# Optimization experiments

Measured on AMD Instinct MI355X. Metric: run time of the kernel, lower is better.

The kernel has to match this reference:

```python
import jax, jax.numpy as jnp
import numpy as np

EMBED_DIM = 1024
NUM_HEADS = 16
HEAD_DIM = EMBED_DIM // NUM_HEADS


def setup_inputs() -> dict:
    key = jax.random.key(0)
    ks = jax.random.split(key, 6)
    s = 1.0 / np.sqrt(EMBED_DIM)
    x = jax.random.normal(ks[0], (2, 2048, EMBED_DIM), dtype=jnp.float32)
    Wk = jax.random.uniform(ks[1], (EMBED_DIM, EMBED_DIM), jnp.float32, -s, s)
    Wq = jax.random.uniform(ks[2], (EMBED_DIM, EMBED_DIM), jnp.float32, -s, s)
    Wv = jax.random.uniform(ks[3], (EMBED_DIM, EMBED_DIM), jnp.float32, -s, s)
    Wo = jax.random.uniform(ks[4], (EMBED_DIM, EMBED_DIM), jnp.float32, -s, s)
    bo = jax.random.uniform(ks[5], (EMBED_DIM,), jnp.float32, -s, s)
    return {"x": x, "Wq": Wq, "Wk": Wk, "Wv": Wv, "Wo": Wo, "bo": bo}


def reference(x, Wq, Wk, Wv, Wo, bo):
    b, s, e = x.shape
    h, d = NUM_HEADS, HEAD_DIM
    scale = d ** (-0.5)
    # nn.Linear: y = x @ W.T ; here W stored as [out, in] -> use W.T
    q = (x @ Wq.T).reshape(b, s, h, d).transpose(0, 2, 1, 3)  # b h s d
    k = (x @ Wk.T).reshape(b, s, h, d).transpose(0, 2, 1, 3)
    v = (x @ Wv.T).reshape(b, s, h, d).transpose(0, 2, 1, 3)
    logits = jnp.einsum('bhqd,bhkd->bhqk', q, k) * scale
    attn = jax.nn.softmax(logits, axis=-1)
    out = jnp.einsum('bhqk,bhkd->bhqd', attn, v)
    out = out.transpose(0, 2, 1, 3).reshape(b, s, e)
    return out @ Wo.T + bo
```

## Files before the change

kernel.cpp:

```cpp
#include <hip/hip_runtime.h>
#include <hip/hip_bf16.h>

using short8 = __attribute__((ext_vector_type(8))) short;
using f32x4  = __attribute__((ext_vector_type(4))) float;
using uint4v = __attribute__((ext_vector_type(4))) unsigned;

#if __has_builtin(__builtin_amdgcn_exp2f)
#define EXP2(x) __builtin_amdgcn_exp2f(x)
#else
#define EXP2(x) exp2f(x)
#endif

__device__ __forceinline__ short f2bf(float f) {
    union { float f; unsigned u; } v; v.f = f;
    unsigned r = v.u + 0x7fffu + ((v.u >> 16) & 1u);
    return (short)(r >> 16);
}
__device__ __forceinline__ unsigned pack_trunc(float a, float b) {
    union { float f; unsigned u; } ua, ub; ua.f = a; ub.f = b;
#if __has_builtin(__builtin_amdgcn_perm)
    return __builtin_amdgcn_perm(ub.u, ua.u, 0x07060302u);
#else
    return (ub.u & 0xFFFF0000u) | (ua.u >> 16);
#endif
}
__device__ __forceinline__ void async_copy16(const short* g, short* s) {
    __builtin_amdgcn_global_load_lds(
        (const __attribute__((address_space(1))) void*)g,
        (__attribute__((address_space(3))) void*)s, 16, 0, 0);
}

__global__ __launch_bounds__(256) void cvt_f32_bf16(
    const float* __restrict__ s0, const float* __restrict__ s1,
    const float* __restrict__ s2, const float* __restrict__ s3,
    const float* __restrict__ s4,
    short* __restrict__ d0, short* __restrict__ d1, short* __restrict__ d2,
    short* __restrict__ d3, short* __restrict__ d4,
    int n0, int n1, int n2, int n3, int n4) {
    const float* s; short* d; int n;
    switch (blockIdx.y) {
        case 0: s = s0; d = d0; n = n0; break;
        case 1: s = s1; d = d1; n = n1; break;
        case 2: s = s2; d = d2; n = n2; break;
        case 3: s = s3; d = d3; n = n3; break;
        default: s = s4; d = d4; n = n4; break;
    }
    const int idx = (blockIdx.x * 256 + threadIdx.x) * 4;
    if (idx < n) {
        float4 v = *(const float4*)(s + idx);
        short4 o;
        o.x = f2bf(v.x); o.y = f2bf(v.y); o.z = f2bf(v.z); o.w = f2bf(v.w);
        *(short4*)(d + idx) = o;
    }
}

template <int MODE, typename OT>
__device__ __forceinline__ void gemm_body(const short* __restrict__ A,
                                          const short* __restrict__ B,
                                          OT* __restrict__ C,
                                          const float* __restrict__ bias,
                                          float scale) {
    constexpr int Kd = 1024, Nd = 1024, Sd = 2048;
    __shared__ __align__(16) short As[128 * 32];
    __shared__ __align__(16) short Bs[128 * 32];

    const int tid  = threadIdx.x;
    const int w    = tid >> 6, lane = tid & 63;
    const int quad = lane >> 4, l16 = lane & 15;
    const int wm   = (w >> 1) * 64, wn = (w & 1) * 64;
    const int bm   = blockIdx.y * 128, bn = blockIdx.x * 128;

    f32x4 acc[4][4];
#pragma unroll
    for (int i = 0; i < 4; ++i)
#pragma unroll
        for (int j = 0; j < 4; ++j) acc[i][j] = (f32x4){0.f, 0.f, 0.f, 0.f};

    for (int k0 = 0; k0 < Kd; k0 += 32) {
        __syncthreads();
#pragma unroll
        for (int c = 0; c < 2; ++c) {
            int li  = c * 256 + tid;
            int row = li >> 2;
            int col = (li & 3) * 8;
            async_copy16(A + (size_t)(bm + row) * Kd + k0 + col, &As[li * 8]);
            async_copy16(B + (size_t)(bn + row) * Kd + k0 + col, &Bs[li * 8]);
        }
        __syncthreads();

        short8 af[4], bfv[4];
#pragma unroll
        for (int mi = 0; mi < 4; ++mi)
            af[mi] = *(const short8*)(&As[(wm + mi * 16 + l16) * 32 + quad * 8]);
#pragma unroll
        for (int ni = 0; ni < 4; ++ni)
            bfv[ni] = *(const short8*)(&Bs[(wn + ni * 16 + l16) * 32 + quad * 8]);
#pragma unroll
        for (int mi = 0; mi < 4; ++mi)
#pragma unroll
            for (int ni = 0; ni < 4; ++ni) {
                if constexpr (MODE == 2)
                    acc[mi][ni] = __builtin_amdgcn_mfma_f32_16x16x32_bf16(
                        bfv[ni], af[mi], acc[mi][ni], 0, 0, 0);
                else
                    acc[mi][ni] = __builtin_amdgcn_mfma_f32_16x16x32_bf16(
                        af[mi], bfv[ni], acc[mi][ni], 0, 0, 0);
            }
    }

    if constexpr (MODE == 2) {
#pragma unroll
        for (int mi = 0; mi < 4; ++mi) {
            const int m_g = bm + wm + mi * 16 + l16;
            const int b_  = m_g >> 11, s_ = m_g & 2047;
#pragma unroll
            for (int ni = 0; ni < 4; ++ni)
#pragma unroll
                for (int r = 0; r < 4; ++r) {
                    const int n_g = bn + wn + ni * 16 + quad * 4 + r;
                    C[(size_t)b_ * Nd * Sd + (size_t)n_g * Sd + s_] =
                        f2bf(acc[mi][ni][r]);
                }
        }
    } else {
#pragma unroll
        for (int ni = 0; ni < 4; ++ni) {
            const int colg = bn + wn + ni * 16 + l16;
            const float bv = (MODE == 1) ? bias[colg] : 0.f;
#pragma unroll
            for (int mi = 0; mi < 4; ++mi)
#pragma unroll
                for (int r = 0; r < 4; ++r) {
                    const int rowg = bm + wm + mi * 16 + quad * 4 + r;
                    if constexpr (MODE == 0)
                        C[(size_t)rowg * Nd + colg] = f2bf(acc[mi][ni][r] * scale);
                    else
                        C[(size_t)rowg * Nd + colg] = acc[mi][ni][r] + bv;
                }
        }
    }
}

#define CSC 0.18033688f

__global__ __launch_bounds__(256, 2) void proj_gemm(
    const short* __restrict__ X,
    const short* __restrict__ Wq, const short* __restrict__ Wk,
    const short* __restrict__ Wv,
    short* __restrict__ Qo, short* __restrict__ Ko, short* __restrict__ VTo) {
    if (blockIdx.z == 0)
        gemm_body<0, short>(X, Wq, Qo, nullptr, CSC);
    else if (blockIdx.z == 1)
        gemm_body<0, short>(X, Wk, Ko, nullptr, 1.0f);
    else
        gemm_body<2, short>(X, Wv, VTo, nullptr, 1.0f);
}

__global__ __launch_bounds__(256, 2) void out_gemm(
    const short* __restrict__ A, const short* __restrict__ W,
    const float* __restrict__ bias, float* __restrict__ C) {
    gemm_body<1, float>(A, W, C, bias, 1.0f);
}

__global__ __launch_bounds__(256, 2) void attn_kernel(
    const short* __restrict__ Q, const short* __restrict__ K,
    const short* __restrict__ VT, short* __restrict__ O) {
    constexpr int S = 2048, E = 1024, NT = S / 64;
    __shared__ __align__(16) short Ks[2][64 * 64];
    __shared__ __align__(16) short Vs[2][64 * 64];

    const int tid  = threadIdx.x;
    const int w    = tid >> 6, lane = tid & 63;
    const int quad = lane >> 4, l16 = lane & 15;
    const int bh   = blockIdx.y, b = bh >> 4, h = bh & 15;
    const int qt   = blockIdx.x;

    const int    q0   = qt * 128 + w * 32;
    const size_t base = (size_t)b * S * E;
    const size_t vtb  = (size_t)b * E * S;
    const int    hc   = h * 64;
    const int    xr   = l16 & 7;

    short8 aq[2][2];
#pragma unroll
    for (int qg = 0; qg < 2; ++qg) {
        const short* qp = Q + base + (size_t)(q0 + qg * 16 + l16) * E + hc + quad * 8;
        aq[qg][0] = *(const short8*)(qp);
        aq[qg][1] = *(const short8*)(qp + 32);
    }

    f32x4 oT[2][4], o_sum[2];
#pragma unroll
    for (int qg = 0; qg < 2; ++qg) {
        o_sum[qg] = (f32x4){0.f, 0.f, 0.f, 0.f};
#pragma unroll
        for (int i = 0; i < 4; ++i) oT[qg][i] = (f32x4){0.f, 0.f, 0.f, 0.f};
    }

    int          kdst[2], vdst0[2], vdst1[2];
    const short* kga[2];
    const short* vga[2];
#pragma unroll
    for (int c = 0; c < 2; ++c) {
        int li = c * 256 + tid, row = li >> 3, cc = li & 7;
        kdst[c] = row * 64 + ((cc ^ (row & 7)) * 8);
        int c0   = 4 * (cc >> 2) + 2 * (cc & 1);
        int boff = 4 * ((cc >> 1) & 1);
        vdst0[c] = row * 64 + ((c0 ^ (row & 7)) * 8) + boff;
        vdst1[c] = row * 64 + (((c0 + 1) ^ (row & 7)) * 8) + boff;
        kga[c]   = K + base + (size_t)row * E + hc + cc * 8;
        vga[c]   = VT + vtb + (size_t)(hc + row) * S + cc * 8;
    }

    short8 kr[2], vr[2];
#pragma unroll
    for (int c = 0; c < 2; ++c) {
        kr[c] = *(const short8*)(kga[c]);
        vr[c] = *(const short8*)(vga[c]);
    }
#pragma unroll
    for (int c = 0; c < 2; ++c) {
        *(short8*)(&Ks[0][kdst[c]]) = kr[c];
        short4 lo, hi;
        lo.x = vr[c][0]; lo.y = vr[c][1]; lo.z = vr[c][2]; lo.w = vr[c][3];
        hi.x = vr[c][4]; hi.y = vr[c][5]; hi.z = vr[c][6]; hi.w = vr[c][7];
        *(short4*)(&Vs[0][vdst0[c]]) = lo;
        *(short4*)(&Vs[0][vdst1[c]]) = hi;
    }
#pragma unroll
    for (int c = 0; c < 2; ++c) {
        kr[c] = *(const short8*)(kga[c] + (size_t)64 * E);
        vr[c] = *(const short8*)(vga[c] + 64);
    }
    __syncthreads();

    const short8 ones = (short8){0x3F80, 0x3F80, 0x3F80, 0x3F80,
                                 0x3F80, 0x3F80, 0x3F80, 0x3F80};
    const float  LB   = 0.00281502f;

    for (int kt = 0; kt < NT; ++kt) {
        const int    cur = kt & 1;
        const short* Kc  = Ks[cur];
        const short* Vc  = Vs[cur];

        if (kt + 1 < NT) {
            short* Kn = Ks[cur ^ 1];
            short* Vn = Vs[cur ^ 1];
#pragma unroll
            for (int c = 0; c < 2; ++c) {
                *(short8*)(&Kn[kdst[c]]) = kr[c];
                short4 lo, hi;
                lo.x = vr[c][0]; lo.y = vr[c][1]; lo.z = vr[c][2]; lo.w = vr[c][3];
                hi.x = vr[c][4]; hi.y = vr[c][5]; hi.z = vr[c][6]; hi.w = vr[c][7];
                *(short4*)(&Vn[vdst0[c]]) = lo;
                *(short4*)(&Vn[vdst1[c]]) = hi;
            }
            if (kt + 2 < NT) {
#pragma unroll
                for (int c = 0; c < 2; ++c) {
                    kr[c] = *(const short8*)(kga[c] + (size_t)(kt + 2) * 64 * E);
                    vr[c] = *(const short8*)(vga[c] + (kt + 2) * 64);
                }
            }
        }

        uint4v pkv[2][2];
#pragma unroll
        for (int kn = 0; kn < 4; ++kn) {
            const short* kb  = &Kc[(kn * 16 + l16) * 64];
            short8       bk0 = *(const short8*)(kb + ((quad ^ xr) * 8));
            short8       bk1 = *(const short8*)(kb + (((quad + 4) ^ xr) * 8));
#pragma unroll
            for (int qg = 0; qg < 2; ++qg) {
                f32x4 a = (f32x4){LB, LB, LB, LB};
                a = __builtin_amdgcn_mfma_f32_16x16x32_bf16(bk0, aq[qg][0], a, 0, 0, 0);
                a = __builtin_amdgcn_mfma_f32_16x16x32_bf16(bk1, aq[qg][1], a, 0, 0, 0);
                pkv[qg][kn >> 1][(kn & 1) * 2]     = pack_trunc(EXP2(a[0]), EXP2(a[1]));
                pkv[qg][kn >> 1][(kn & 1) * 2 + 1] = pack_trunc(EXP2(a[2]), EXP2(a[3]));
            }
        }

#pragma unroll
        for (int ks = 0; ks < 2; ++ks) {
            short8 pf[2];
#pragma unroll
            for (int qg = 0; qg < 2; ++qg) {
                union { uint4v u; short8 s; } cv;
                cv.u   = pkv[qg][ks];
                pf[qg] = cv.s;
                o_sum[qg] = __builtin_amdgcn_mfma_f32_16x16x32_bf16(
                    ones, pf[qg], o_sum[qg], 0, 0, 0);
            }
#pragma unroll
            for (int ni = 0; ni < 4; ++ni) {
                const int rv = ni * 16 + l16;
                short8 vb =
                    *(const short8*)(&Vc[rv * 64 + (((ks * 4 + quad) ^ xr) * 8)]);
#pragma unroll
                for (int qg = 0; qg < 2; ++qg)
                    oT[qg][ni] = __builtin_amdgcn_mfma_f32_16x16x32_bf16(
                        vb, pf[qg], oT[qg][ni], 0, 0, 0);
            }
        }
        __syncthreads();
    }

#pragma unroll
    for (int qg = 0; qg < 2; ++qg) {
        const float inv = 1.0f / o_sum[qg][0];
        const int   qg_ = q0 + qg * 16 + l16;
#pragma unroll
        for (int ni = 0; ni < 4; ++ni) {
            short4 ov;
            ov.x = f2bf(oT[qg][ni][0] * inv);
            ov.y = f2bf(oT[qg][ni][1] * inv);
            ov.z = f2bf(oT[qg][ni][2] * inv);
            ov.w = f2bf(oT[qg][ni][3] * inv);
            *(short4*)(&O[base + (size_t)qg_ * E + hc + ni * 16 + quad * 4]) = ov;
        }
    }
}

extern "C" void kernel_launch(void* const* d_in, const int* in_sizes, int n_in,
                              void* d_out, int out_size, void* d_ws, size_t ws_size,
                              hipStream_t stream) {
    const float* x  = (const float*)d_in[0];
    const float* Wq = (const float*)d_in[1];
    const float* Wk = (const float*)d_in[2];
    const float* Wv = (const float*)d_in[3];
    const float* Wo = (const float*)d_in[4];
    const float* bo = (const float*)d_in[5];
    float* out = (float*)d_out;

    constexpr int XN = 2 * 2048 * 1024;
    constexpr int WN = 1024 * 1024;

    short* Xb  = (short*)d_ws;
    short* Wqb = Xb + XN;
    short* Wkb = Wqb + WN;
    short* Wvb = Wkb + WN;
    short* Wob = Wvb + WN;
    short* Qb  = Wob + WN;
    short* Kb  = Qb + XN;
    short* VTb = Kb + XN;

    cvt_f32_bf16<<<dim3(4096, 5), 256, 0, stream>>>(
        x, Wq, Wk, Wv, Wo, Xb, Wqb, Wkb, Wvb, Wob, XN, WN, WN, WN, WN);
    proj_gemm<<<dim3(8, 32, 3), 256, 0, stream>>>(Xb, Wqb, Wkb, Wvb, Qb, Kb, VTb);
    attn_kernel<<<dim3(16, 32), 256, 0, stream>>>(Qb, Kb, VTb, Xb );
    out_gemm<<<dim3(8, 32, 1), 256, 0, stream>>>(Xb, Wob, bo, out);
}
```

Baseline: 178.9 us.

## Widen per-wave query tile in attention and retile output GEMM to 64x128

```diff
diff --git a/kernel.cpp b/kernel.cpp
--- a/kernel.cpp
+++ b/kernel.cpp
@@ -54,11 +54,10 @@
     }
 }
 
-template <int MODE, typename OT>
+template <int MODE>
 __device__ __forceinline__ void gemm_body(const short* __restrict__ A,
                                           const short* __restrict__ B,
-                                          OT* __restrict__ C,
-                                          const float* __restrict__ bias,
+                                          short* __restrict__ C,
                                           float scale) {
     constexpr int Kd = 1024, Nd = 1024, Sd = 2048;
     __shared__ __align__(16) short As[128 * 32];
@@ -126,16 +125,12 @@
 #pragma unroll
         for (int ni = 0; ni < 4; ++ni) {
             const int colg = bn + wn + ni * 16 + l16;
-            const float bv = (MODE == 1) ? bias[colg] : 0.f;
 #pragma unroll
             for (int mi = 0; mi < 4; ++mi)
 #pragma unroll
                 for (int r = 0; r < 4; ++r) {
                     const int rowg = bm + wm + mi * 16 + quad * 4 + r;
-                    if constexpr (MODE == 0)
-                        C[(size_t)rowg * Nd + colg] = f2bf(acc[mi][ni][r] * scale);
-                    else
-                        C[(size_t)rowg * Nd + colg] = acc[mi][ni][r] + bv;
+                    C[(size_t)rowg * Nd + colg] = f2bf(acc[mi][ni][r] * scale);
                 }
         }
     }
@@ -149,20 +144,77 @@
     const short* __restrict__ Wv,
     short* __restrict__ Qo, short* __restrict__ Ko, short* __restrict__ VTo) {
     if (blockIdx.z == 0)
-        gemm_body<0, short>(X, Wq, Qo, nullptr, CSC);
+        gemm_body<0>(X, Wq, Qo, CSC);
     else if (blockIdx.z == 1)
-        gemm_body<0, short>(X, Wk, Ko, nullptr, 1.0f);
+        gemm_body<0>(X, Wk, Ko, 1.0f);
     else
-        gemm_body<2, short>(X, Wv, VTo, nullptr, 1.0f);
+        gemm_body<2>(X, Wv, VTo, 1.0f);
 }
 
 __global__ __launch_bounds__(256, 2) void out_gemm(
-    const short* __restrict__ A, const short* __restrict__ W,
+    const short* __restrict__ A, const short* __restrict__ B,
     const float* __restrict__ bias, float* __restrict__ C) {
-    gemm_body<1, float>(A, W, C, bias, 1.0f);
-}
-
-__global__ __launch_bounds__(256, 2) void attn_kernel(
+    constexpr int Kd = 1024, Nd = 1024;
+    __shared__ __align__(16) short As[64 * 32];
+    __shared__ __align__(16) short Bs[128 * 32];
+
+    const int tid  = threadIdx.x;
+    const int w    = tid >> 6, lane = tid & 63;
+    const int quad = lane >> 4, l16 = lane & 15;
+    const int wm   = (w >> 1) * 32, wn = (w & 1) * 64;
+    const int bm   = blockIdx.y * 64, bn = blockIdx.x * 128;
+
+    f32x4 acc[2][4];
+#pragma unroll
+    for (int i = 0; i < 2; ++i)
+#pragma unroll
+        for (int j = 0; j < 4; ++j) acc[i][j] = (f32x4){0.f, 0.f, 0.f, 0.f};
+
+    for (int k0 = 0; k0 < Kd; k0 += 32) {
+        __syncthreads();
+        {
+            int row = tid >> 2, col = (tid & 3) * 8;
+            async_copy16(A + (size_t)(bm + row) * Kd + k0 + col, &As[tid * 8]);
+        }
+#pragma unroll
+        for (int c = 0; c < 2; ++c) {
+            int li  = c * 256 + tid;
+            int row = li >> 2;
+            int col = (li & 3) * 8;
+            async_copy16(B + (size_t)(bn + row) * Kd + k0 + col, &Bs[li * 8]);
+        }
+        __syncthreads();
+
+        short8 af[2], bfv[4];
+#pragma unroll
+        for (int mi = 0; mi < 2; ++mi)
+            af[mi] = *(const short8*)(&As[(wm + mi * 16 + l16) * 32 + quad * 8]);
+#pragma unroll
+        for (int ni = 0; ni < 4; ++ni)
+            bfv[ni] = *(const short8*)(&Bs[(wn + ni * 16 + l16) * 32 + quad * 8]);
+#pragma unroll
+        for (int mi = 0; mi < 2; ++mi)
+#pragma unroll
+            for (int ni = 0; ni < 4; ++ni)
+                acc[mi][ni] = __builtin_amdgcn_mfma_f32_16x16x32_bf16(
+                    af[mi], bfv[ni], acc[mi][ni], 0, 0, 0);
+    }
+
+#pragma unroll
+    for (int ni = 0; ni < 4; ++ni) {
+        const int colg = bn + wn + ni * 16 + l16;
+        const float bv = bias[colg];
+#pragma unroll
+        for (int mi = 0; mi < 2; ++mi)
+#pragma unroll
+            for (int r = 0; r < 4; ++r) {
+                const int rowg = bm + wm + mi * 16 + quad * 4 + r;
+                C[(size_t)rowg * Nd + colg] = acc[mi][ni][r] + bv;
+            }
+    }
+}
+
+__global__ __launch_bounds__(128, 1) void attn_kernel(
     const short* __restrict__ Q, const short* __restrict__ K,
     const short* __restrict__ VT, short* __restrict__ O) {
     constexpr int S = 2048, E = 1024, NT = S / 64;
@@ -175,34 +227,34 @@
     const int bh   = blockIdx.y, b = bh >> 4, h = bh & 15;
     const int qt   = blockIdx.x;
 
-    const int    q0   = qt * 128 + w * 32;
+    const int    q0   = qt * 128 + w * 64;
     const size_t base = (size_t)b * S * E;
     const size_t vtb  = (size_t)b * E * S;
     const int    hc   = h * 64;
     const int    xr   = l16 & 7;
 
-    short8 aq[2][2];
-#pragma unroll
-    for (int qg = 0; qg < 2; ++qg) {
+    short8 aq[4][2];
+#pragma unroll
+    for (int qg = 0; qg < 4; ++qg) {
         const short* qp = Q + base + (size_t)(q0 + qg * 16 + l16) * E + hc + quad * 8;
         aq[qg][0] = *(const short8*)(qp);
         aq[qg][1] = *(const short8*)(qp + 32);
     }
 
-    f32x4 oT[2][4], o_sum[2];
-#pragma unroll
-    for (int qg = 0; qg < 2; ++qg) {
+    f32x4 oT[4][4], o_sum[4];
+#pragma unroll
+    for (int qg = 0; qg < 4; ++qg) {
         o_sum[qg] = (f32x4){0.f, 0.f, 0.f, 0.f};
 #pragma unroll
         for (int i = 0; i < 4; ++i) oT[qg][i] = (f32x4){0.f, 0.f, 0.f, 0.f};
     }
 
-    int          kdst[2], vdst0[2], vdst1[2];
-    const short* kga[2];
-    const short* vga[2];
-#pragma unroll
-    for (int c = 0; c < 2; ++c) {
-        int li = c * 256 + tid, row = li >> 3, cc = li & 7;
+    int          kdst[4], vdst0[4], vdst1[4];
+    const short* kga[4];
+    const short* vga[4];
+#pragma unroll
+    for (int c = 0; c < 4; ++c) {
+        int li = c * 128 + tid, row = li >> 3, cc = li & 7;
         kdst[c] = row * 64 + ((cc ^ (row & 7)) * 8);
         int c0   = 4 * (cc >> 2) + 2 * (cc & 1);
         int boff = 4 * ((cc >> 1) & 1);
@@ -212,14 +264,14 @@
         vga[c]   = VT + vtb + (size_t)(hc + row) * S + cc * 8;
     }
 
-    short8 kr[2], vr[2];
-#pragma unroll
-    for (int c = 0; c < 2; ++c) {
+    short8 kr[4], vr[4];
+#pragma unroll
+    for (int c = 0; c < 4; ++c) {
         kr[c] = *(const short8*)(kga[c]);
         vr[c] = *(const short8*)(vga[c]);
     }
 #pragma unroll
-    for (int c = 0; c < 2; ++c) {
+    for (int c = 0; c < 4; ++c) {
         *(short8*)(&Ks[0][kdst[c]]) = kr[c];
         short4 lo, hi;
         lo.x = vr[c][0]; lo.y = vr[c][1]; lo.z = vr[c][2]; lo.w = vr[c][3];
@@ -228,7 +280,7 @@
         *(short4*)(&Vs[0][vdst1[c]]) = hi;
     }
 #pragma unroll
-    for (int c = 0; c < 2; ++c) {
+    for (int c = 0; c < 4; ++c) {
         kr[c] = *(const short8*)(kga[c] + (size_t)64 * E);
         vr[c] = *(const short8*)(vga[c] + 64);
     }
@@ -247,7 +299,7 @@
             short* Kn = Ks[cur ^ 1];
             short* Vn = Vs[cur ^ 1];
 #pragma unroll
-            for (int c = 0; c < 2; ++c) {
+            for (int c = 0; c < 4; ++c) {
                 *(short8*)(&Kn[kdst[c]]) = kr[c];
                 short4 lo, hi;
                 lo.x = vr[c][0]; lo.y = vr[c][1]; lo.z = vr[c][2]; lo.w = vr[c][3];
@@ -257,21 +309,21 @@
             }
             if (kt + 2 < NT) {
 #pragma unroll
-                for (int c = 0; c < 2; ++c) {
+                for (int c = 0; c < 4; ++c) {
                     kr[c] = *(const short8*)(kga[c] + (size_t)(kt + 2) * 64 * E);
                     vr[c] = *(const short8*)(vga[c] + (kt + 2) * 64);
                 }
             }
         }
 
-        uint4v pkv[2][2];
+        uint4v pkv[4][2];
 #pragma unroll
         for (int kn = 0; kn < 4; ++kn) {
             const short* kb  = &Kc[(kn * 16 + l16) * 64];
             short8       bk0 = *(const short8*)(kb + ((quad ^ xr) * 8));
             short8       bk1 = *(const short8*)(kb + (((quad + 4) ^ xr) * 8));
 #pragma unroll
-            for (int qg = 0; qg < 2; ++qg) {
+            for (int qg = 0; qg < 4; ++qg) {
                 f32x4 a = (f32x4){LB, LB, LB, LB};
                 a = __builtin_amdgcn_mfma_f32_16x16x32_bf16(bk0, aq[qg][0], a, 0, 0, 0);
                 a = __builtin_amdgcn_mfma_f32_16x16x32_bf16(bk1, aq[qg][1], a, 0, 0, 0);
@@ -282,9 +334,9 @@
 
 #pragma unroll
         for (int ks = 0; ks < 2; ++ks) {
-            short8 pf[2];
-#pragma unroll
-            for (int qg = 0; qg < 2; ++qg) {
+            short8 pf[4];
+#pragma unroll
+            for (int qg = 0; qg < 4; ++qg) {
                 union { uint4v u; short8 s; } cv;
                 cv.u   = pkv[qg][ks];
                 pf[qg] = cv.s;
@@ -297,7 +349,7 @@
                 short8 vb =
                     *(const short8*)(&Vc[rv * 64 + (((ks * 4 + quad) ^ xr) * 8)]);
 #pragma unroll
-                for (int qg = 0; qg < 2; ++qg)
+                for (int qg = 0; qg < 4; ++qg)
                     oT[qg][ni] = __builtin_amdgcn_mfma_f32_16x16x32_bf16(
                         vb, pf[qg], oT[qg][ni], 0, 0, 0);
             }
@@ -306,7 +358,7 @@
     }
 
 #pragma unroll
-    for (int qg = 0; qg < 2; ++qg) {
+    for (int qg = 0; qg < 4; ++qg) {
         const float inv = 1.0f / o_sum[qg][0];
         const int   qg_ = q0 + qg * 16 + l16;
 #pragma unroll
@@ -347,6 +399,6 @@
     cvt_f32_bf16<<<dim3(4096, 5), 256, 0, stream>>>(
         x, Wq, Wk, Wv, Wo, Xb, Wqb, Wkb, Wvb, Wob, XN, WN, WN, WN, WN);
     proj_gemm<<<dim3(8, 32, 3), 256, 0, stream>>>(Xb, Wqb, Wkb, Wvb, Qb, Kb, VTb);
-    attn_kernel<<<dim3(16, 32), 256, 0, stream>>>(Qb, Kb, VTb, Xb );
-    out_gemm<<<dim3(8, 32, 1), 256, 0, stream>>>(Xb, Wob, bo, out);
-}
+    attn_kernel<<<dim3(16, 32), 128, 0, stream>>>(Qb, Kb, VTb, Xb );
+    out_gemm<<<dim3(8, 64), 256, 0, stream>>>(Xb, Wob, bo, out);
+}
```

New measurement: 191.5 us. 7.1% more time.
